# Optimization experiments

Measured on AMD Instinct MI355X. Metric: run time of the kernel, lower is better.

## Reference

```python
import jax, jax.numpy as jnp
import numpy as np

N, IN, OUT, H, ED, E = 50000, 128, 128, 3, 16, 800000
NEG_SLOPE = 0.2
LN_EPS = 1e-5


def setup_inputs() -> dict:
    key = jax.random.key(0)
    ks = jax.random.split(key, 12)
    s = lambda k, shape, fan: jax.random.normal(k, shape, jnp.float32) / np.sqrt(fan)
    return {
        "x": jax.random.normal(ks[0], (N, IN), jnp.float32),
        "edge_index": jax.random.randint(ks[1], (2, E), 0, N, jnp.int64),
        "edge_attr": jax.random.normal(ks[2], (E, ED), jnp.float32),
        # GATConv params
        "W": s(ks[3], (IN, H * OUT), IN),          # lin_src (shared src/dst), bias=False
        "W_edge": s(ks[4], (ED, H * OUT), ED),     # lin_edge, bias=False
        "att_src": s(ks[5], (H, OUT), OUT),
        "att_dst": s(ks[6], (H, OUT), OUT),
        "att_edge": s(ks[7], (H, OUT), OUT),
        "gat_bias": jnp.zeros((H * OUT,), jnp.float32),
        # trailing Linear + LayerNorm
        "lin_W": s(ks[8], (H * OUT, OUT), H * OUT),
        "lin_b": jnp.zeros((OUT,), jnp.float32),
        "ln_g": jnp.ones((OUT,), jnp.float32),
        "ln_b": jnp.zeros((OUT,), jnp.float32),
    }


def gat_block(x, edge_index, edge_attr, W, W_edge, att_src, att_dst, att_edge,
              gat_bias, lin_W, lin_b, ln_g, ln_b):
    row, col = edge_index[0], edge_index[1]
    n = x.shape[0]

    # add_self_loops with fill_value='mean': per-dst mean of incoming edge_attr
    deg = jax.ops.segment_sum(jnp.ones((edge_attr.shape[0],), x.dtype), col, num_segments=n)
    loop_attr = jax.ops.segment_sum(edge_attr, col, num_segments=n) / jnp.maximum(deg, 1.0)[:, None]
    loop = jnp.arange(n, dtype=row.dtype)
    row2 = jnp.concatenate([row, loop])
    col2 = jnp.concatenate([col, loop])
    ea2 = jnp.concatenate([edge_attr, loop_attr], axis=0)

    xp = (x @ W).reshape(n, H, OUT)                       # [N,H,C]
    a_src = jnp.einsum('nhc,hc->nh', xp, att_src)         # [N,H]
    a_dst = jnp.einsum('nhc,hc->nh', xp, att_dst)
    ep = (ea2 @ W_edge).reshape(-1, H, OUT)               # [E2,H,C]
    a_edge = jnp.einsum('ehc,hc->eh', ep, att_edge)

    alpha = a_src[row2] + a_dst[col2] + a_edge            # [E2,H]
    alpha = jnp.where(alpha >= 0, alpha, NEG_SLOPE * alpha)

    # segment softmax over destination nodes
    m = jax.ops.segment_max(alpha, col2, num_segments=n)
    ex = jnp.exp(alpha - m[col2])
    denom = jax.ops.segment_sum(ex, col2, num_segments=n)
    attn = ex / denom[col2]                               # [E2,H]

    msg = attn[:, :, None] * xp[row2]                     # [E2,H,C]
    agg = jax.ops.segment_sum(msg, col2, num_segments=n)  # [N,H,C]
    x_gat = agg.reshape(n, H * OUT) + gat_bias

    y = x_gat @ lin_W + lin_b                             # [N,OUT]
    h = x + y
    mu = h.mean(-1, keepdims=True)
    var = ((h - mu) ** 2).mean(-1, keepdims=True)
    return (h - mu) * jax.lax.rsqrt(var + LN_EPS) * ln_g + ln_b


def reference(x, edge_index, edge_attr, W, W_edge, att_src, att_dst, att_edge,
              gat_bias, lin_W, lin_b, ln_g, ln_b):
    return gat_block(x, edge_index, edge_attr, W, W_edge, att_src, att_dst,
                     att_edge, gat_bias, lin_W, lin_b, ln_g, ln_b)
```

## Files before the change

### kernel.cpp

```cpp
#include <hip/hip_runtime.h>
#include <hip/hip_bf16.h>
#include <math.h>

#define M_NODES 50000
#define IN_F    128
#define OUT_F   128
#define NH      3
#define ED_F    16
#define NE      800000
#define HO      (NH * OUT_F)
#define NEG_SLOPE 0.2f
#define LN_EPS    1e-5f
#define CAP     64

#define PB_ATTN 782
#define PB_FILL (PB_ATTN + 3125)
#define PB_PQ   (PB_FILL + 192)
#define PB_TOT  (PB_PQ + 1)

typedef __attribute__((ext_vector_type(8))) short bf16x8;
typedef __attribute__((ext_vector_type(4))) float f32x4;

__device__ __forceinline__ float b2f(unsigned short u) {
    unsigned int x = ((unsigned int)u) << 16;
    return __uint_as_float(x);
}
__device__ __forceinline__ unsigned short f2b(float f) {
    __hip_bfloat16 h = __float2bfloat16(f);
    return *(unsigned short*)&h;
}

__global__ __launch_bounds__(64)
void k_small(const float* __restrict__ W, const float* __restrict__ Wed,
             const float* __restrict__ a_s, const float* __restrict__ a_d,
             const float* __restrict__ a_e, float* __restrict__ small)
{
    int o = blockIdx.x, l = threadIdx.x;
    if (o < 384) {
        int k = o / 3, h = o - k * 3;
        float wA = W[(size_t)k * HO + h * 128 + l];
        float wB = W[(size_t)k * HO + h * 128 + 64 + l];
        float s1 = wA * a_s[h * 128 + l] + wB * a_s[h * 128 + 64 + l];
        float s2 = wA * a_d[h * 128 + l] + wB * a_d[h * 128 + 64 + l];
        #pragma unroll
        for (int s = 32; s; s >>= 1) { s1 += __shfl_xor(s1, s); s2 += __shfl_xor(s2, s); }
        if (l == 0) { small[h * 128 + k] = s1; small[384 + h * 128 + k] = s2; }
    } else {
        int u = o - 384;
        int d = u / 3, h = u - d * 3;
        float s = Wed[(size_t)d * HO + h * 128 + l] * a_e[h * 128 + l]
                + Wed[(size_t)d * HO + h * 128 + 64 + l] * a_e[h * 128 + 64 + l];
        #pragma unroll
        for (int ss = 32; ss; ss >>= 1) s += __shfl_xor(s, ss);
        if (l == 0) small[768 + u] = s;
    }
}

__global__ __launch_bounds__(256)
void k_pre(const float* __restrict__ x, const float* __restrict__ W,
           const float* __restrict__ lw, const float* __restrict__ gb,
           const float* __restrict__ lb, const int* __restrict__ ei,
           const float* __restrict__ ea, const float* __restrict__ small,
           float4* __restrict__ asrc4, float4* __restrict__ adst4,
           unsigned short* __restrict__ x16, int* __restrict__ cursor,
           float4* __restrict__ edata,
           unsigned short* __restrict__ Qt, float* __restrict__ b2)
{
    int b = blockIdx.x, t = threadIdx.x;
    if (b < PB_ATTN) {
        __shared__ float smp[24 * 36];
        for (int i = t; i < 768; i += 256) {
            int s = i >> 9;
            s = i / 384;
            int rem = i - s * 384;
            int h = rem >> 7, rem2 = rem & 127;
            int j = rem2 >> 5, col = rem2 & 31;
            smp[(s * 12 + h * 4 + j) * 36 + col] = small[i];
        }
        __syncthreads();
        int g = t >> 2, j = t & 3;
        int n = b * 64 + g;
        if (n < M_NODES) {
            const float4* xr = (const float4*)x + (size_t)n * 32 + j * 8;
            float4 xv[8];
            #pragma unroll
            for (int i = 0; i < 8; ++i) xv[i] = xr[i];
            unsigned int pk[16];
            #pragma unroll
            for (int i = 0; i < 8; ++i) {
                pk[2*i]   = (unsigned int)f2b(xv[i].x) | ((unsigned int)f2b(xv[i].y) << 16);
                pk[2*i+1] = (unsigned int)f2b(xv[i].z) | ((unsigned int)f2b(xv[i].w) << 16);
            }
            uint4* xo = (uint4*)(x16 + (size_t)n * IN_F + j * 32);
            xo[0] = make_uint4(pk[0],  pk[1],  pk[2],  pk[3]);
            xo[1] = make_uint4(pk[4],  pk[5],  pk[6],  pk[7]);
            xo[2] = make_uint4(pk[8],  pk[9],  pk[10], pk[11]);
            xo[3] = make_uint4(pk[12], pk[13], pk[14], pk[15]);
            float p[3] = {0.f,0.f,0.f}, q[3] = {0.f,0.f,0.f};
            #pragma unroll
            for (int i = 0; i < 8; ++i) {
                float4 v = xv[i];
                #pragma unroll
                for (int h = 0; h < 3; ++h) {
                    float4 ws = *(const float4*)&smp[(h * 4 + j) * 36 + i * 4];
                    float4 wd = *(const float4*)&smp[(12 + h * 4 + j) * 36 + i * 4];
                    p[h] += v.x * ws.x + v.y * ws.y + v.z * ws.z + v.w * ws.w;
                    q[h] += v.x * wd.x + v.y * wd.y + v.z * wd.z + v.w * wd.w;
                }
            }
            #pragma unroll
            for (int h = 0; h < 3; ++h) {
                p[h] += __shfl_xor(p[h], 1); p[h] += __shfl_xor(p[h], 2);
                q[h] += __shfl_xor(q[h], 1); q[h] += __shfl_xor(q[h], 2);
            }
            if (j == 0) {
                asrc4[n] = make_float4(p[0], p[1], p[2], 0.f);
                adst4[n] = make_float4(q[0], q[1], q[2], 0.f);
            }
        }
    } else if (b < PB_FILL) {
        int e = (b - PB_ATTN) * 256 + t;
        int r = ei[e], c = ei[NE + e];
        const float4* p = (const float4*)(ea + (size_t)e * 16);
        float4 q0 = p[0], q1 = p[1], q2 = p[2], q3 = p[3];
        float v[16] = {q0.x,q0.y,q0.z,q0.w, q1.x,q1.y,q1.z,q1.w,
                       q2.x,q2.y,q2.z,q2.w, q3.x,q3.y,q3.z,q3.w};
        const float* Wev = small + 768;
        float ae[3];
        #pragma unroll
        for (int h = 0; h < 3; ++h) {
            float s = 0.f;
            #pragma unroll
            for (int d = 0; d < 16; ++d) s += v[d] * Wev[d * 3 + h];
            ae[h] = s;
        }
        int pos = atomicAdd(&cursor[c], 1);
        if (pos < CAP)
            edata[(size_t)c * CAP + pos] = make_float4(__int_as_float(r), ae[0], ae[1], ae[2]);
    } else if (b < PB_PQ) {
        int i = (b - PB_FILL) * 2 + (t >> 7);
        int h = i >> 7, tt = i & 127;
        int j = t & 127;
        float s = 0.f;
        const float* wrow = W + (size_t)tt * HO + h * 128;
        const float* lcol = lw + (size_t)(h * 128) * 128 + j;
        #pragma unroll 4
        for (int c = 0; c < 128; ++c)
            s += wrow[c] * lcol[(size_t)c * 128];
        Qt[(size_t)j * HO + i] = f2b(s);
    } else {
        if (t < 128) {
            int j = t;
            float s0 = lb[j], s1 = 0.f, s2 = 0.f, s3 = 0.f;
            for (int i = 0; i < HO; i += 4) {
                s0 += gb[i]     * lw[(size_t)i * 128 + j];
                s1 += gb[i + 1] * lw[(size_t)(i + 1) * 128 + j];
                s2 += gb[i + 2] * lw[(size_t)(i + 2) * 128 + j];
                s3 += gb[i + 3] * lw[(size_t)(i + 3) * 128 + j];
            }
            b2[j] = s0 + s1 + s2 + s3;
        }
    }
}

__global__ __launch_bounds__(256)
void k_agg(const int* __restrict__ cursor, const float4* __restrict__ edata,
           const float4* __restrict__ asrc4, const float4* __restrict__ adst4,
           const unsigned short* __restrict__ x16, unsigned short* __restrict__ sbar)
{
    __shared__ float4 wsh[4][64];
    int t = threadIdx.x;
    int wv = t >> 6, l = t & 63;
    int n = blockIdx.x * 4 + wv;
    int ne_raw = cursor[n];
    int ne = ne_raw < CAP ? ne_raw : CAP;
    float4 ad = adst4[n];
    int h = l >> 5, q = l & 31;
    const char* xb = (const char*)x16;

    float a0[4] = {0.f,0.f,0.f,0.f};
    float a1[4] = {0.f,0.f,0.f,0.f};
    float a2[4] = {0.f,0.f,0.f,0.f};
    float pd0=0.f, pd1=0.f, pd2=0.f, pa0=0.f, pa1=0.f, pa2=0.f;

    if (l < ne) {
        float4 m0 = edata[(size_t)n * CAP + l];
        int r = __float_as_int(m0.x);
        float4 as = asrc4[r];
        float al0 = m0.y + as.x + ad.x;
        float al1 = m0.z + as.y + ad.y;
        float al2 = m0.w + as.z + ad.z;
        al0 = (al0 >= 0.f) ? al0 : NEG_SLOPE * al0;
        al1 = (al1 >= 0.f) ? al1 : NEG_SLOPE * al1;
        al2 = (al2 >= 0.f) ? al2 : NEG_SLOPE * al2;
        float w0 = __expf(al0), w1 = __expf(al1), w2 = __expf(al2);
        pa0 = m0.y; pa1 = m0.z; pa2 = m0.w;
        pd0 = w0; pd1 = w1; pd2 = w2;
        wsh[wv][l] = make_float4(w0, w1, w2, m0.x);
    }
    asm volatile("s_waitcnt lgkmcnt(0)" ::: "memory");
    __builtin_amdgcn_sched_barrier(0);
    #pragma unroll 2
    for (int i = h; i < ne; i += 2) {
        float4 m = wsh[wv][i];
        int r = __float_as_int(m.w);
        uint2 v = *(const uint2*)(xb + (size_t)r * 256 + q * 8);
        float e0 = __uint_as_float(v.x << 16);
        float e1 = __uint_as_float(v.x & 0xFFFF0000u);
        float e2 = __uint_as_float(v.y << 16);
        float e3 = __uint_as_float(v.y & 0xFFFF0000u);
        a0[0] += m.x * e0; a0[1] += m.x * e1; a0[2] += m.x * e2; a0[3] += m.x * e3;
        a1[0] += m.y * e0; a1[1] += m.y * e1; a1[2] += m.y * e2; a1[3] += m.y * e3;
        a2[0] += m.z * e0; a2[1] += m.z * e1; a2[2] += m.z * e2; a2[3] += m.z * e3;
    }

    #pragma unroll
    for (int j = 0; j < 4; ++j) {
        a0[j] += __shfl_xor(a0[j], 32);
        a1[j] += __shfl_xor(a1[j], 32);
        a2[j] += __shfl_xor(a2[j], 32);
    }
    #pragma unroll
    for (int s = 32; s; s >>= 1) {
        pd0 += __shfl_xor(pd0, s); pd1 += __shfl_xor(pd1, s); pd2 += __shfl_xor(pd2, s);
        pa0 += __shfl_xor(pa0, s); pa1 += __shfl_xor(pa1, s); pa2 += __shfl_xor(pa2, s);
    }

    float4 as = asrc4[n];
    float inv = 1.0f / fmaxf((float)ne_raw, 1.0f);
    float al0 = as.x + ad.x + pa0 * inv;
    float al1 = as.y + ad.y + pa1 * inv;
    float al2 = as.z + ad.z + pa2 * inv;
    al0 = (al0 >= 0.f) ? al0 : NEG_SLOPE * al0;
    al1 = (al1 >= 0.f) ? al1 : NEG_SLOPE * al1;
    al2 = (al2 >= 0.f) ? al2 : NEG_SLOPE * al2;
    float w0 = __expf(al0), w1 = __expf(al1), w2 = __expf(al2);
    float d0 = pd0 + w0, d1 = pd1 + w1, d2 = pd2 + w2;
    float i0 = 1.f / d0, i1 = 1.f / d1, i2 = 1.f / d2;

    if (l < 32) {
        uint2 xv = *(const uint2*)(xb + (size_t)n * 256 + q * 8);
        float e0 = __uint_as_float(xv.x << 16);
        float e1 = __uint_as_float(xv.x & 0xFFFF0000u);
        float e2 = __uint_as_float(xv.y << 16);
        float e3 = __uint_as_float(xv.y & 0xFFFF0000u);
        uint2* ob = (uint2*)(sbar + (size_t)n * HO);
        unsigned int p0, p1;
        p0 = (unsigned int)f2b((a0[0] + w0 * e0) * i0) | ((unsigned int)f2b((a0[1] + w0 * e1) * i0) << 16);
        p1 = (unsigned int)f2b((a0[2] + w0 * e2) * i0) | ((unsigned int)f2b((a0[3] + w0 * e3) * i0) << 16);
        ob[q] = make_uint2(p0, p1);
        p0 = (unsigned int)f2b((a1[0] + w1 * e0) * i1) | ((unsigned int)f2b((a1[1] + w1 * e1) * i1) << 16);
        p1 = (unsigned int)f2b((a1[2] + w1 * e2) * i1) | ((unsigned int)f2b((a1[3] + w1 * e3) * i1) << 16);
        ob[32 + q] = make_uint2(p0, p1);
        p0 = (unsigned int)f2b((a2[0] + w2 * e0) * i2) | ((unsigned int)f2b((a2[1] + w2 * e1) * i2) << 16);
        p1 = (unsigned int)f2b((a2[2] + w2 * e2) * i2) | ((unsigned int)f2b((a2[3] + w2 * e3) * i2) << 16);
        ob[64 + q] = make_uint2(p0, p1);
    }
}

__global__ __launch_bounds__(256)
void k_mm2_ln(const unsigned short* __restrict__ A, const unsigned short* __restrict__ Bt,
              const float* __restrict__ bias, const float* __restrict__ xres,
              const float* __restrict__ lng, const float* __restrict__ lnb,
              float* __restrict__ out)
{
    __shared__ char lds[24576];
    const int bm = blockIdx.x * 64;
    const int tid = threadIdx.x, w = tid >> 6, lane = tid & 63;
    const int lrow = lane & 15, lk = lane >> 4;
    const short z0 = 0;
    f32x4 acc[8];
    #pragma unroll
    for (int f = 0; f < 8; ++f) { acc[f][0]=0.f; acc[f][1]=0.f; acc[f][2]=0.f; acc[f][3]=0.f; }

    for (int k0 = 0; k0 < 384; k0 += 64) {
        #pragma unroll
        for (int it = 0; it < 2; ++it) {
            int c = tid + it * 256;
            int row = c >> 3, o = c & 7;
            int grow = bm + row;
            bf16x8 v = {z0,z0,z0,z0,z0,z0,z0,z0};
            if (grow < M_NODES) v = *(const bf16x8*)(A + (size_t)grow * 384 + k0 + o * 8);
            int b = (row * 128 + o * 16) ^ ((row & 7) << 4);
            *(bf16x8*)(lds + b) = v;
        }
        #pragma unroll
        for (int it = 0; it < 4; ++it) {
            int c = tid + it * 256;
            int row = c >> 3, o = c & 7;
            bf16x8 v = *(const bf16x8*)(Bt + (size_t)row * 384 + k0 + o * 8);
            int b = 8192 + ((row * 128 + o * 16) ^ ((row & 7) << 4));
            *(bf16x8*)(lds + b) = v;
        }
        __syncthreads();
        #pragma unroll
        for (int kk = 0; kk < 2; ++kk) {
            int ar = w * 16 + lrow;
            bf16x8 a = *(const bf16x8*)(lds + ((ar * 128 + kk * 64 + lk * 16) ^ ((lrow & 7) << 4)));
            #pragma unroll
            for (int f = 0; f < 8; ++f) {
                int br = 16 * f + lrow;
                bf16x8 bb = *(const bf16x8*)(lds + 8192 + ((br * 128 + kk * 64 + lk * 16) ^ ((lrow & 7) << 4)));
                acc[f] = __builtin_amdgcn_mfma_f32_16x16x32_bf16(a, bb, acc[f], 0, 0, 0);
            }
        }
        __syncthreads();
    }

    int cols[8]; float bs[8], gg[8], bbv[8];
    #pragma unroll
    for (int f = 0; f < 8; ++f) {
        cols[f] = 16 * f + lrow;
        bs[f] = bias[cols[f]];
        gg[f] = lng[cols[f]];
        bbv[f] = lnb[cols[f]];
    }
    #pragma unroll
    for (int rg = 0; rg < 4; ++rg) {
        int grow = bm + w * 16 + lk * 4 + rg;
        bool ok = grow < M_NODES;
        float h[8];
        float s = 0.f;
        #pragma unroll
        for (int f = 0; f < 8; ++f) {
            float hv = 0.f;
            if (ok) hv = acc[f][rg] + bs[f] + xres[(size_t)grow * 128 + cols[f]];
            h[f] = hv;
            s += hv;
        }
        #pragma unroll
        for (int m = 1; m < 16; m <<= 1) s += __shfl_xor(s, m);
        float mu = s * (1.0f / 128.0f);
        float vv = 0.f;
        #pragma unroll
        for (int f = 0; f < 8; ++f) { float d = h[f] - mu; vv += d * d; }
        #pragma unroll
        for (int m = 1; m < 16; m <<= 1) vv += __shfl_xor(vv, m);
        float rs = rsqrtf(vv * (1.0f / 128.0f) + LN_EPS);
        if (ok) {
            #pragma unroll
            for (int f = 0; f < 8; ++f)
                out[(size_t)grow * 128 + cols[f]] = (h[f] - mu) * rs * gg[f] + bbv[f];
        }
    }
}

extern "C" void kernel_launch(void* const* d_in, const int* in_sizes, int n_in,
                              void* d_out, int out_size, void* d_ws, size_t ws_size,
                              hipStream_t stream)
{
    const float* x    = (const float*)d_in[0];
    const int*   ei   = (const int*)  d_in[1];
    const float* ea   = (const float*)d_in[2];
    const float* W    = (const float*)d_in[3];
    const float* Wed  = (const float*)d_in[4];
    const float* asv  = (const float*)d_in[5];
    const float* adv  = (const float*)d_in[6];
    const float* aev  = (const float*)d_in[7];
    const float* gb   = (const float*)d_in[8];
    const float* lw   = (const float*)d_in[9];
    const float* lb   = (const float*)d_in[10];
    const float* lng  = (const float*)d_in[11];
    const float* lnb  = (const float*)d_in[12];
    float* out = (float*)d_out;

    char* wsp = (char*)d_ws;
    size_t off = 0;
    auto alloc = [&](size_t bytes) -> void* {
        void* p = wsp + off;
        off += bytes;
        off = (off + 255) & ~(size_t)255;
        return p;
    };

    int*   cursor  = (int*)  alloc((size_t)M_NODES * 4);
    size_t zero_bytes = off;
    float* small   = (float*)alloc(816 * 4);
    float* b2      = (float*)alloc(128 * 4);
    float4* asrc4  = (float4*)alloc((size_t)M_NODES * 16);
    float4* adst4  = (float4*)alloc((size_t)M_NODES * 16);
    float4* edata  = (float4*)alloc((size_t)M_NODES * CAP * 16);
    unsigned short* x16   = (unsigned short*)alloc((size_t)M_NODES * IN_F * 2);
    unsigned short* Qt16  = (unsigned short*)alloc((size_t)OUT_F * HO * 2);
    unsigned short* sbar  = (unsigned short*)alloc((size_t)M_NODES * HO * 2);
    (void)ws_size; (void)in_sizes; (void)n_in; (void)out_size;

    hipMemsetAsync(d_ws, 0, zero_bytes, stream);

    k_small<<<432, 64, 0, stream>>>(W, Wed, asv, adv, aev, small);
    k_pre<<<PB_TOT, 256, 0, stream>>>(x, W, lw, gb, lb, ei, ea, small,
                                      asrc4, adst4, x16, cursor, edata, Qt16, b2);
    k_agg<<<M_NODES / 4, 256, 0, stream>>>(cursor, edata, asrc4, adst4, x16, sbar);
    k_mm2_ln<<<(M_NODES + 63) / 64, 256, 0, stream>>>(sbar, Qt16, b2, x, lng, lnb, out);
}
```

Before: 136.7 us.

## Replace global-atomic edge bucketing with two-pass binned counting sort

Edge scattering into per-destination slots no longer uses global atomics on a cursor array. The fill stage now writes edge records to a linear buffer and bins edge ids by destination group (256 nodes per bin) using shared-memory atomics. A new sort kernel then gathers each bin's entries and places them with shared-memory atomics, which also removes the memset. This adds a kernel launch plus extra global traffic (aebuf, binbuf, and a strided cntbuf read), and it silently drops edges when more than 16 from one block land in a single bin.

Measured after the change: 159.6 us. +16.8%, slower.

```diff
diff --git a/kernel.cpp b/kernel.cpp
--- a/kernel.cpp
+++ b/kernel.cpp
@@ -12,9 +12,12 @@
 #define NEG_SLOPE 0.2f
 #define LN_EPS    1e-5f
 #define CAP     64
+#define NBIN    196
+#define NFB     3125
+#define BCAP    16
 
 #define PB_ATTN 782
-#define PB_FILL (PB_ATTN + 3125)
+#define PB_FILL (PB_ATTN + NFB)
 #define PB_PQ   (PB_FILL + 192)
 #define PB_TOT  (PB_PQ + 1)
 
@@ -62,16 +65,15 @@
            const float* __restrict__ lb, const int* __restrict__ ei,
            const float* __restrict__ ea, const float* __restrict__ small,
            float4* __restrict__ asrc4, float4* __restrict__ adst4,
-           unsigned short* __restrict__ x16, int* __restrict__ cursor,
-           float4* __restrict__ edata,
+           unsigned short* __restrict__ x16, float4* __restrict__ aebuf4,
+           unsigned int* __restrict__ binbuf, unsigned char* __restrict__ cntbuf,
            unsigned short* __restrict__ Qt, float* __restrict__ b2)
 {
     int b = blockIdx.x, t = threadIdx.x;
     if (b < PB_ATTN) {
         __shared__ float smp[24 * 36];
         for (int i = t; i < 768; i += 256) {
-            int s = i >> 9;
-            s = i / 384;
+            int s = i / 384;
             int rem = i - s * 384;
             int h = rem >> 7, rem2 = rem & 127;
             int j = rem2 >> 5, col = rem2 & 31;
@@ -119,7 +121,11 @@
             }
         }
     } else if (b < PB_FILL) {
-        int e = (b - PB_ATTN) * 256 + t;
+        __shared__ int binrun[NBIN];
+        int blk = b - PB_ATTN;
+        if (t < NBIN) binrun[t] = 0;
+        __syncthreads();
+        int e = blk * 256 + t;
         int r = ei[e], c = ei[NE + e];
         const float4* p = (const float4*)(ea + (size_t)e * 16);
         float4 q0 = p[0], q1 = p[1], q2 = p[2], q3 = p[3];
@@ -134,9 +140,14 @@
             for (int d = 0; d < 16; ++d) s += v[d] * Wev[d * 3 + h];
             ae[h] = s;
         }
-        int pos = atomicAdd(&cursor[c], 1);
-        if (pos < CAP)
-            edata[(size_t)c * CAP + pos] = make_float4(__int_as_float(r), ae[0], ae[1], ae[2]);
+        aebuf4[e] = make_float4(__int_as_float(r), ae[0], ae[1], ae[2]);
+        int bin = c >> 8;
+        int rank = atomicAdd(&binrun[bin], 1);
+        if (rank < BCAP)
+            binbuf[((size_t)bin * NFB + blk) * BCAP + rank] =
+                ((unsigned int)e << 8) | (unsigned int)(c & 255);
+        __syncthreads();
+        if (t < NBIN) cntbuf[(size_t)blk * NBIN + t] = (unsigned char)binrun[t];
     } else if (b < PB_PQ) {
         int i = (b - PB_FILL) * 2 + (t >> 7);
         int h = i >> 7, tt = i & 127;
@@ -163,6 +174,40 @@
     }
 }
 
+__global__ __launch_bounds__(1024)
+void k_sort(const unsigned int* __restrict__ binbuf,
+            const unsigned char* __restrict__ cntbuf,
+            const float4* __restrict__ aebuf4,
+            int* __restrict__ cursor, float4* __restrict__ edata)
+{
+    __shared__ int run[256];
+    __shared__ unsigned char cnts[NFB];
+    int bin = blockIdx.x, t = threadIdx.x;
+    if (t < 256) run[t] = 0;
+    for (int i = t; i < NFB; i += 1024)
+        cnts[i] = cntbuf[(size_t)i * NBIN + bin];
+    __syncthreads();
+    const unsigned int* bb = binbuf + (size_t)bin * NFB * BCAP;
+    for (int i = t; i < NFB * BCAP; i += 1024) {
+        int blk = i >> 4, s = i & 15;
+        if (s < (int)cnts[blk]) {
+            unsigned int v = bb[i];
+            int cl = v & 255;
+            unsigned int e = v >> 8;
+            float4 rec = aebuf4[e];
+            int rank = atomicAdd(&run[cl], 1);
+            int c = (bin << 8) + cl;
+            if (rank < CAP)
+                edata[(size_t)c * CAP + rank] = rec;
+        }
+    }
+    __syncthreads();
+    if (t < 256) {
+        int n = (bin << 8) + t;
+        if (n < M_NODES) cursor[n] = run[t];
+    }
+}
+
 __global__ __launch_bounds__(256)
 void k_agg(const int* __restrict__ cursor, const float4* __restrict__ edata,
            const float4* __restrict__ asrc4, const float4* __restrict__ adst4,
@@ -373,23 +418,25 @@
         return p;
     };
 
-    int*   cursor  = (int*)  alloc((size_t)M_NODES * 4);
-    size_t zero_bytes = off;
     float* small   = (float*)alloc(816 * 4);
     float* b2      = (float*)alloc(128 * 4);
+    int*   cursor  = (int*)  alloc((size_t)M_NODES * 4);
     float4* asrc4  = (float4*)alloc((size_t)M_NODES * 16);
     float4* adst4  = (float4*)alloc((size_t)M_NODES * 16);
+    float4* aebuf4 = (float4*)alloc((size_t)NE * 16);
+    unsigned int*  binbuf = (unsigned int*)alloc((size_t)NBIN * NFB * BCAP * 4);
+    unsigned char* cntbuf = (unsigned char*)alloc((size_t)NFB * NBIN);
     float4* edata  = (float4*)alloc((size_t)M_NODES * CAP * 16);
     unsigned short* x16   = (unsigned short*)alloc((size_t)M_NODES * IN_F * 2);
     unsigned short* Qt16  = (unsigned short*)alloc((size_t)OUT_F * HO * 2);
     unsigned short* sbar  = (unsigned short*)alloc((size_t)M_NODES * HO * 2);
     (void)ws_size; (void)in_sizes; (void)n_in; (void)out_size;
 
-    hipMemsetAsync(d_ws, 0, zero_bytes, stream);
 
     k_small<<<432, 64, 0, stream>>>(W, Wed, asv, adv, aev, small);
     k_pre<<<PB_TOT, 256, 0, stream>>>(x, W, lw, gb, lb, ei, ea, small,
-                                      asrc4, adst4, x16, cursor, edata, Qt16, b2);
+                                      asrc4, adst4, x16, aebuf4, binbuf, cntbuf, Qt16, b2);
+    k_sort<<<NBIN, 1024, 0, stream>>>(binbuf, cntbuf, aebuf4, cursor, edata);
     k_agg<<<M_NODES / 4, 256, 0, stream>>>(cursor, edata, asrc4, adst4, x16, sbar);
     k_mm2_ln<<<(M_NODES + 63) / 64, 256, 0, stream>>>(sbar, Qt16, b2, x, lng, lnb, out);
 }
```

## Map one node per half-wave in aggregation and parallelize bias reduction

Applied to the files above, without the earlier changes.

The aggregation kernel now handles two destination nodes per wavefront, one per 32-lane half, instead of one node per full wave with the edges split across the halves. This removes the cross-half shuffle reduction of the accumulators, halves the block count, and keeps all lanes busy in the epilogue, but each half-wave now walks its node's edges serially. The fused bias vector is now computed by 128 blocks with block reductions instead of one block looping serially. The edge-fill branch issues its atomic earlier and writes records with nontemporal stores.

New measurement: 132.1 us. -3.3%, faster.

```diff
diff --git a/kernel.cpp b/kernel.cpp
--- a/kernel.cpp
+++ b/kernel.cpp
@@ -16,7 +16,7 @@
 #define PB_ATTN 782
 #define PB_FILL (PB_ATTN + 3125)
 #define PB_PQ   (PB_FILL + 192)
-#define PB_TOT  (PB_PQ + 1)
+#define PB_TOT  (PB_PQ + 128)
 
 typedef __attribute__((ext_vector_type(8))) short bf16x8;
 typedef __attribute__((ext_vector_type(4))) float f32x4;
@@ -70,8 +70,7 @@
     if (b < PB_ATTN) {
         __shared__ float smp[24 * 36];
         for (int i = t; i < 768; i += 256) {
-            int s = i >> 9;
-            s = i / 384;
+            int s = i / 384;
             int rem = i - s * 384;
             int h = rem >> 7, rem2 = rem & 127;
             int j = rem2 >> 5, col = rem2 & 31;
@@ -80,47 +79,47 @@
         __syncthreads();
         int g = t >> 2, j = t & 3;
         int n = b * 64 + g;
-        if (n < M_NODES) {
-            const float4* xr = (const float4*)x + (size_t)n * 32 + j * 8;
-            float4 xv[8];
-            #pragma unroll
-            for (int i = 0; i < 8; ++i) xv[i] = xr[i];
-            unsigned int pk[16];
-            #pragma unroll
-            for (int i = 0; i < 8; ++i) {
-                pk[2*i]   = (unsigned int)f2b(xv[i].x) | ((unsigned int)f2b(xv[i].y) << 16);
-                pk[2*i+1] = (unsigned int)f2b(xv[i].z) | ((unsigned int)f2b(xv[i].w) << 16);
-            }
-            uint4* xo = (uint4*)(x16 + (size_t)n * IN_F + j * 32);
-            xo[0] = make_uint4(pk[0],  pk[1],  pk[2],  pk[3]);
-            xo[1] = make_uint4(pk[4],  pk[5],  pk[6],  pk[7]);
-            xo[2] = make_uint4(pk[8],  pk[9],  pk[10], pk[11]);
-            xo[3] = make_uint4(pk[12], pk[13], pk[14], pk[15]);
-            float p[3] = {0.f,0.f,0.f}, q[3] = {0.f,0.f,0.f};
-            #pragma unroll
-            for (int i = 0; i < 8; ++i) {
-                float4 v = xv[i];
-                #pragma unroll
-                for (int h = 0; h < 3; ++h) {
-                    float4 ws = *(const float4*)&smp[(h * 4 + j) * 36 + i * 4];
-                    float4 wd = *(const float4*)&smp[(12 + h * 4 + j) * 36 + i * 4];
-                    p[h] += v.x * ws.x + v.y * ws.y + v.z * ws.z + v.w * ws.w;
-                    q[h] += v.x * wd.x + v.y * wd.y + v.z * wd.z + v.w * wd.w;
-                }
-            }
+        if (n >= M_NODES) return;
+        const float4* xr = (const float4*)x + (size_t)n * 32 + j * 8;
+        float4 xv[8];
+        #pragma unroll
+        for (int i = 0; i < 8; ++i) xv[i] = xr[i];
+        unsigned int pk[16];
+        #pragma unroll
+        for (int i = 0; i < 8; ++i) {
+            pk[2*i]   = (unsigned int)f2b(xv[i].x) | ((unsigned int)f2b(xv[i].y) << 16);
+            pk[2*i+1] = (unsigned int)f2b(xv[i].z) | ((unsigned int)f2b(xv[i].w) << 16);
+        }
+        uint4* xo = (uint4*)(x16 + (size_t)n * IN_F + j * 32);
+        xo[0] = make_uint4(pk[0],  pk[1],  pk[2],  pk[3]);
+        xo[1] = make_uint4(pk[4],  pk[5],  pk[6],  pk[7]);
+        xo[2] = make_uint4(pk[8],  pk[9],  pk[10], pk[11]);
+        xo[3] = make_uint4(pk[12], pk[13], pk[14], pk[15]);
+        float p[3] = {0.f,0.f,0.f}, q[3] = {0.f,0.f,0.f};
+        #pragma unroll
+        for (int i = 0; i < 8; ++i) {
+            float4 v = xv[i];
             #pragma unroll
             for (int h = 0; h < 3; ++h) {
-                p[h] += __shfl_xor(p[h], 1); p[h] += __shfl_xor(p[h], 2);
-                q[h] += __shfl_xor(q[h], 1); q[h] += __shfl_xor(q[h], 2);
+                float4 ws = *(const float4*)&smp[(h * 4 + j) * 36 + i * 4];
+                float4 wd = *(const float4*)&smp[(12 + h * 4 + j) * 36 + i * 4];
+                p[h] += v.x * ws.x + v.y * ws.y + v.z * ws.z + v.w * ws.w;
+                q[h] += v.x * wd.x + v.y * wd.y + v.z * wd.z + v.w * wd.w;
             }
-            if (j == 0) {
-                asrc4[n] = make_float4(p[0], p[1], p[2], 0.f);
-                adst4[n] = make_float4(q[0], q[1], q[2], 0.f);
-            }
+        }
+        #pragma unroll
+        for (int h = 0; h < 3; ++h) {
+            p[h] += __shfl_xor(p[h], 1); p[h] += __shfl_xor(p[h], 2);
+            q[h] += __shfl_xor(q[h], 1); q[h] += __shfl_xor(q[h], 2);
+        }
+        if (j == 0) {
+            asrc4[n] = make_float4(p[0], p[1], p[2], 0.f);
+            adst4[n] = make_float4(q[0], q[1], q[2], 0.f);
         }
     } else if (b < PB_FILL) {
         int e = (b - PB_ATTN) * 256 + t;
         int r = ei[e], c = ei[NE + e];
+        int pos = atomicAdd(&cursor[c], 1);
         const float4* p = (const float4*)(ea + (size_t)e * 16);
         float4 q0 = p[0], q1 = p[1], q2 = p[2], q3 = p[3];
         float v[16] = {q0.x,q0.y,q0.z,q0.w, q1.x,q1.y,q1.z,q1.w,
@@ -134,9 +133,11 @@
             for (int d = 0; d < 16; ++d) s += v[d] * Wev[d * 3 + h];
             ae[h] = s;
         }
-        int pos = atomicAdd(&cursor[c], 1);
-        if (pos < CAP)
-            edata[(size_t)c * CAP + pos] = make_float4(__int_as_float(r), ae[0], ae[1], ae[2]);
+        if (pos < CAP) {
+            f32x4 rec;
+            rec[0] = __int_as_float(r); rec[1] = ae[0]; rec[2] = ae[1]; rec[3] = ae[2];
+            __builtin_nontemporal_store(rec, (f32x4*)&edata[(size_t)c * CAP + pos]);
+        }
     } else if (b < PB_PQ) {
         int i = (b - PB_FILL) * 2 + (t >> 7);
         int h = i >> 7, tt = i & 127;
@@ -149,17 +150,16 @@
             s += wrow[c] * lcol[(size_t)c * 128];
         Qt[(size_t)j * HO + i] = f2b(s);
     } else {
-        if (t < 128) {
-            int j = t;
-            float s0 = lb[j], s1 = 0.f, s2 = 0.f, s3 = 0.f;
-            for (int i = 0; i < HO; i += 4) {
-                s0 += gb[i]     * lw[(size_t)i * 128 + j];
-                s1 += gb[i + 1] * lw[(size_t)(i + 1) * 128 + j];
-                s2 += gb[i + 2] * lw[(size_t)(i + 2) * 128 + j];
-                s3 += gb[i + 3] * lw[(size_t)(i + 3) * 128 + j];
-            }
-            b2[j] = s0 + s1 + s2 + s3;
-        }
+        __shared__ float red[4];
+        int j = b - PB_PQ;
+        float s = 0.f;
+        for (int i = t; i < HO; i += 256) s += gb[i] * lw[(size_t)i * 128 + j];
+        #pragma unroll
+        for (int k = 32; k; k >>= 1) s += __shfl_xor(s, k);
+        int w = t >> 6, lane = t & 63;
+        if (lane == 0) red[w] = s;
+        __syncthreads();
+        if (t == 0) b2[j] = lb[j] + red[0] + red[1] + red[2] + red[3];
     }
 }
 
@@ -168,14 +168,14 @@
            const float4* __restrict__ asrc4, const float4* __restrict__ adst4,
            const unsigned short* __restrict__ x16, unsigned short* __restrict__ sbar)
 {
-    __shared__ float4 wsh[4][64];
+    __shared__ float4 wsh[4][2][CAP];
     int t = threadIdx.x;
     int wv = t >> 6, l = t & 63;
-    int n = blockIdx.x * 4 + wv;
+    int h = l >> 5, q = l & 31;
+    int n = blockIdx.x * 8 + wv * 2 + h;
     int ne_raw = cursor[n];
     int ne = ne_raw < CAP ? ne_raw : CAP;
     float4 ad = adst4[n];
-    int h = l >> 5, q = l & 31;
     const char* xb = (const char*)x16;
 
     float a0[4] = {0.f,0.f,0.f,0.f};
@@ -183,26 +183,37 @@
     float a2[4] = {0.f,0.f,0.f,0.f};
     float pd0=0.f, pd1=0.f, pd2=0.f, pa0=0.f, pa1=0.f, pa2=0.f;
 
-    if (l < ne) {
-        float4 m0 = edata[(size_t)n * CAP + l];
-        int r = __float_as_int(m0.x);
-        float4 as = asrc4[r];
-        float al0 = m0.y + as.x + ad.x;
-        float al1 = m0.z + as.y + ad.y;
-        float al2 = m0.w + as.z + ad.z;
-        al0 = (al0 >= 0.f) ? al0 : NEG_SLOPE * al0;
-        al1 = (al1 >= 0.f) ? al1 : NEG_SLOPE * al1;
-        al2 = (al2 >= 0.f) ? al2 : NEG_SLOPE * al2;
-        float w0 = __expf(al0), w1 = __expf(al1), w2 = __expf(al2);
-        pa0 = m0.y; pa1 = m0.z; pa2 = m0.w;
-        pd0 = w0; pd1 = w1; pd2 = w2;
-        wsh[wv][l] = make_float4(w0, w1, w2, m0.x);
+    #pragma unroll
+    for (int base = 0; base < CAP; base += 32) {
+        int i = base + q;
+        if (i < ne) {
+            float4 m0 = edata[(size_t)n * CAP + i];
+            int r = __float_as_int(m0.x);
+            float4 as = asrc4[r];
+            float al0 = m0.y + as.x + ad.x;
+            float al1 = m0.z + as.y + ad.y;
+            float al2 = m0.w + as.z + ad.z;
+            al0 = (al0 >= 0.f) ? al0 : NEG_SLOPE * al0;
+            al1 = (al1 >= 0.f) ? al1 : NEG_SLOPE * al1;
+            al2 = (al2 >= 0.f) ? al2 : NEG_SLOPE * al2;
+            float w0 = __expf(al0), w1 = __expf(al1), w2 = __expf(al2);
+            pa0 += m0.y; pa1 += m0.z; pa2 += m0.w;
+            pd0 += w0; pd1 += w1; pd2 += w2;
+            wsh[wv][h][i] = make_float4(w0, w1, w2, m0.x);
+        }
     }
     asm volatile("s_waitcnt lgkmcnt(0)" ::: "memory");
     __builtin_amdgcn_sched_barrier(0);
+
+    #pragma unroll
+    for (int s = 16; s; s >>= 1) {
+        pd0 += __shfl_xor(pd0, s); pd1 += __shfl_xor(pd1, s); pd2 += __shfl_xor(pd2, s);
+        pa0 += __shfl_xor(pa0, s); pa1 += __shfl_xor(pa1, s); pa2 += __shfl_xor(pa2, s);
+    }
+
     #pragma unroll 2
-    for (int i = h; i < ne; i += 2) {
-        float4 m = wsh[wv][i];
+    for (int i = 0; i < ne; ++i) {
+        float4 m = wsh[wv][h][i];
         int r = __float_as_int(m.w);
         uint2 v = *(const uint2*)(xb + (size_t)r * 256 + q * 8);
         float e0 = __uint_as_float(v.x << 16);
@@ -212,18 +223,6 @@
         a0[0] += m.x * e0; a0[1] += m.x * e1; a0[2] += m.x * e2; a0[3] += m.x * e3;
         a1[0] += m.y * e0; a1[1] += m.y * e1; a1[2] += m.y * e2; a1[3] += m.y * e3;
         a2[0] += m.z * e0; a2[1] += m.z * e1; a2[2] += m.z * e2; a2[3] += m.z * e3;
-    }
-
-    #pragma unroll
-    for (int j = 0; j < 4; ++j) {
-        a0[j] += __shfl_xor(a0[j], 32);
-        a1[j] += __shfl_xor(a1[j], 32);
-        a2[j] += __shfl_xor(a2[j], 32);
-    }
-    #pragma unroll
-    for (int s = 32; s; s >>= 1) {
-        pd0 += __shfl_xor(pd0, s); pd1 += __shfl_xor(pd1, s); pd2 += __shfl_xor(pd2, s);
-        pa0 += __shfl_xor(pa0, s); pa1 += __shfl_xor(pa1, s); pa2 += __shfl_xor(pa2, s);
     }
 
     float4 as = asrc4[n];
@@ -238,24 +237,22 @@
     float d0 = pd0 + w0, d1 = pd1 + w1, d2 = pd2 + w2;
     float i0 = 1.f / d0, i1 = 1.f / d1, i2 = 1.f / d2;
 
-    if (l < 32) {
-        uint2 xv = *(const uint2*)(xb + (size_t)n * 256 + q * 8);
-        float e0 = __uint_as_float(xv.x << 16);
-        float e1 = __uint_as_float(xv.x & 0xFFFF0000u);
-        float e2 = __uint_as_float(xv.y << 16);
-        float e3 = __uint_as_float(xv.y & 0xFFFF0000u);
-        uint2* ob = (uint2*)(sbar + (size_t)n * HO);
-        unsigned int p0, p1;
-        p0 = (unsigned int)f2b((a0[0] + w0 * e0) * i0) | ((unsigned int)f2b((a0[1] + w0 * e1) * i0) << 16);
-        p1 = (unsigned int)f2b((a0[2] + w0 * e2) * i0) | ((unsigned int)f2b((a0[3] + w0 * e3) * i0) << 16);
-        ob[q] = make_uint2(p0, p1);
-        p0 = (unsigned int)f2b((a1[0] + w1 * e0) * i1) | ((unsigned int)f2b((a1[1] + w1 * e1) * i1) << 16);
-        p1 = (unsigned int)f2b((a1[2] + w1 * e2) * i1) | ((unsigned int)f2b((a1[3] + w1 * e3) * i1) << 16);
-        ob[32 + q] = make_uint2(p0, p1);
-        p0 = (unsigned int)f2b((a2[0] + w2 * e0) * i2) | ((unsigned int)f2b((a2[1] + w2 * e1) * i2) << 16);
-        p1 = (unsigned int)f2b((a2[2] + w2 * e2) * i2) | ((unsigned int)f2b((a2[3] + w2 * e3) * i2) << 16);
-        ob[64 + q] = make_uint2(p0, p1);
-    }
+    uint2 xv = *(const uint2*)(xb + (size_t)n * 256 + q * 8);
+    float e0 = __uint_as_float(xv.x << 16);
+    float e1 = __uint_as_float(xv.x & 0xFFFF0000u);
+    float e2 = __uint_as_float(xv.y << 16);
+    float e3 = __uint_as_float(xv.y & 0xFFFF0000u);
+    uint2* ob = (uint2*)(sbar + (size_t)n * HO);
+    unsigned int p0, p1;
+    p0 = (unsigned int)f2b((a0[0] + w0 * e0) * i0) | ((unsigned int)f2b((a0[1] + w0 * e1) * i0) << 16);
+    p1 = (unsigned int)f2b((a0[2] + w0 * e2) * i0) | ((unsigned int)f2b((a0[3] + w0 * e3) * i0) << 16);
+    ob[q] = make_uint2(p0, p1);
+    p0 = (unsigned int)f2b((a1[0] + w1 * e0) * i1) | ((unsigned int)f2b((a1[1] + w1 * e1) * i1) << 16);
+    p1 = (unsigned int)f2b((a1[2] + w1 * e2) * i1) | ((unsigned int)f2b((a1[3] + w1 * e3) * i1) << 16);
+    ob[32 + q] = make_uint2(p0, p1);
+    p0 = (unsigned int)f2b((a2[0] + w2 * e0) * i2) | ((unsigned int)f2b((a2[1] + w2 * e1) * i2) << 16);
+    p1 = (unsigned int)f2b((a2[2] + w2 * e2) * i2) | ((unsigned int)f2b((a2[3] + w2 * e3) * i2) << 16);
+    ob[64 + q] = make_uint2(p0, p1);
 }
 
 __global__ __launch_bounds__(256)
@@ -385,11 +382,11 @@
     unsigned short* sbar  = (unsigned short*)alloc((size_t)M_NODES * HO * 2);
     (void)ws_size; (void)in_sizes; (void)n_in; (void)out_size;
 
-    hipMemsetAsync(d_ws, 0, zero_bytes, stream);
+    (void)hipMemsetAsync(d_ws, 0, zero_bytes, stream);
 
     k_small<<<432, 64, 0, stream>>>(W, Wed, asv, adv, aev, small);
     k_pre<<<PB_TOT, 256, 0, stream>>>(x, W, lw, gb, lb, ei, ea, small,
                                       asrc4, adst4, x16, cursor, edata, Qt16, b2);
-    k_agg<<<M_NODES / 4, 256, 0, stream>>>(cursor, edata, asrc4, adst4, x16, sbar);
+    k_agg<<<M_NODES / 8, 256, 0, stream>>>(cursor, edata, asrc4, adst4, x16, sbar);
     k_mm2_ln<<<(M_NODES + 63) / 64, 256, 0, stream>>>(sbar, Qt16, b2, x, lng, lnb, out);
 }
```
